# Kernel optimization log

Hardware: AMD Instinct MI355X
Metric: run time of the kernel (lower is better)

Reference implementation:

```python
import jax, jax.numpy as jnp
import numpy as np

EPS = 1e-8
NU_MOLECULAR = 1.5e-05
# loss weights (module defaults)
DATA_W, BC_W, TURB_W, RANS_W, SMOOTH_W, WALL_W = 1.0, 0.05, 0.05, 0.05, 0.01, 0.02
CONT_INIT = CONT_TGT = 0.1
MOM_INIT = MOM_TGT = 0.1
RAMP_STEPS, RAMP_START = 1000, 0

N_NODES, N_EDGES = 100000, 6400000


def _curriculum_weights(step):
    if step < RAMP_START:
        return CONT_INIT, MOM_INIT
    if step >= RAMP_START + RAMP_STEPS:
        return CONT_TGT, MOM_TGT
    alpha = (step - RAMP_START) / RAMP_STEPS  # linear ramp
    return ((1 - alpha) * CONT_INIT + alpha * CONT_TGT,
            (1 - alpha) * MOM_INIT + alpha * MOM_TGT)


def setup_inputs() -> dict:
    key = jax.random.key(0)
    k1, k2, k3, k4, k5 = jax.random.split(key, 5)
    predictions = jax.random.normal(k1, (N_NODES, 4), dtype=jnp.float32)
    targets = jax.random.normal(k2, (N_NODES, 4), dtype=jnp.float32)
    # dx, dy strictly positive edge offsets
    edge_attr_dxdy = jax.random.uniform(k3, (N_EDGES, 2), dtype=jnp.float32, minval=1e-3, maxval=0.05)
    edge_index = jax.random.randint(k4, (2, N_EDGES), 0, N_NODES, dtype=jnp.int64)
    wall_mask = jax.random.bernoulli(k5, 0.05, (N_NODES,))
    return {"predictions": predictions, "targets": targets,
            "edge_attr_dxdy": edge_attr_dxdy, "edge_index": edge_index,
            "wall_mask": wall_mask, "step": 500}


def reference(predictions, targets, edge_attr_dxdy, edge_index, wall_mask, step):
    cont_w, mom_w = _curriculum_weights(int(step))
    N = predictions.shape[0]
    row, col = edge_index[0], edge_index[1]
    u, v, p, nu_t = (predictions[:, i] for i in range(4))
    dx, dy = edge_attr_dxdy[:, 0], edge_attr_dxdy[:, 1]

    # per-edge finite differences (single gather of node fields)
    du = u[col] - u[row]
    dv = v[col] - v[row]
    dp = p[col] - p[row]

    seg = lambda e: jax.ops.segment_sum(e, row, num_segments=N)
    edge_count = jnp.maximum(seg(jnp.ones_like(du)), 1.0)

    # --- data loss ---
    mse_loss = jnp.mean((predictions - targets) ** 2)

    # --- continuity (divergence) loss ---
    divergence = (seg(du / (dx + EPS)) + seg(dv / (dy + EPS))) / edge_count
    div_loss = jnp.mean(divergence ** 2)

    # --- momentum loss ---
    p_grad_x = seg(dp / (dx + EPS)) / edge_count
    p_grad_y = seg(dp / (dy + EPS)) / edge_count
    lap_u = seg(du / (dx ** 2 + EPS)) / edge_count
    lap_v = seg(dv / (dy ** 2 + EPS)) / edge_count
    nu_eff = NU_MOLECULAR + nu_t
    momentum_loss = jnp.mean((p_grad_x + nu_eff * lap_u) ** 2 +
                             (p_grad_y + nu_eff * lap_v) ** 2)

    # --- turbulence losses ---
    positivity_loss = jnp.mean(jax.nn.relu(-nu_t) ** 2)
    du_dx = du / (dx + EPS)
    du_dy = du / (dy + EPS)
    dv_dx = dv / (dx + EPS)
    dv_dy = dv / (dy + EPS)
    strain_sq_edge = 2.0 * (du_dx ** 2 + dv_dy ** 2) + (du_dy + dv_dx) ** 2
    strain_node = seg(strain_sq_edge) / edge_count
    production = nu_t * strain_node
    turb_production_loss = jnp.mean(production ** 2)
    turb_dissipation_loss = jnp.mean(nu_t ** 2)

    # --- boundary-condition & wall-function losses (wall mask) ---
    m = wall_mask.astype(u.dtype)
    n_wall = jnp.maximum(jnp.sum(m), 1.0)
    bc_loss = jnp.sum(m * (u ** 2 + v ** 2)) / n_wall
    wall_loss = jnp.sum(m * (u ** 2 + v ** 2 + nu_t ** 2)) / n_wall

    # --- smoothness loss over edges ---
    smooth_loss = jnp.mean((predictions[col] - predictions[row]) ** 2)

    total = (DATA_W * mse_loss + cont_w * div_loss + mom_w * momentum_loss +
             TURB_W * turb_production_loss + RANS_W * turb_dissipation_loss +
             BC_W * bc_loss + SMOOTH_W * smooth_loss + WALL_W * wall_loss)
    # positivity_loss is tracked but not weighted into total (per visible code paths)
    return total
```

## Files before the change

### kernel.cpp

```cpp
#include <hip/hip_runtime.h>
#include <hip/hip_fp16.h>

#define EPS 1e-8f
#define NU_MOL 1.5e-5f
#define NPB 512
#define MAXNB 256
#define NBP 256
#define NBLK 4096
#define CMAX 1664
#define KMAX 7
#define CH 2048
#define SPLIT 6
#define NGRP 64
#define GRP 64


union U32H2 { unsigned u; __half2 h; };

__device__ inline unsigned packh2(float a, float b) {
    U32H2 x; x.h = __halves2half2(__float2half_rn(a), __float2half_rn(b));
    return x.u;
}
__device__ inline float2 unpackh2(unsigned u) {
    U32H2 x; x.u = u;
    return make_float2(__low2float(x.h), __high2float(x.h));
}
__device__ inline unsigned bf16rne(float f) {
    unsigned u = __float_as_uint(f);
    u += 0x7FFFu + ((u >> 16) & 1u);
    return u >> 16;
}
__device__ inline float bf16dec(unsigned h) {
    return __uint_as_float(h << 16);
}


__global__ void detect_idx_dtype(const void* eidx, int N, int* flag) {
    const long long* ll = (const long long*)eidx;
    int is64 = 1;
    for (int i = 0; i < 16; ++i) {
        long long v = ll[i];
        if (v < 0 || v >= (long long)N) { is64 = 0; break; }
    }
    *flag = is64;
}

__global__ void finalize_kernel(const double* __restrict__ d,
                                const double* __restrict__ smooth_slots,
                                int N, int E, float* __restrict__ out)
{
    double smooth = 0.0;
    for (int i = 0; i < 64; ++i) smooth += smooth_slots[i];
    double dN = (double)N;
    double n_wall = d[5] > 1.0 ? d[5] : 1.0;
    double total = 1.0  * d[0] / (4.0 * dN)
                 + 0.1  * d[1] / dN
                 + 0.1  * d[2] / dN
                 + 0.05 * d[3] / dN
                 + 0.05 * d[4] / dN
                 + 0.05 * d[6] / n_wall
                 + 0.01 * smooth / (4.0 * (double)E)
                 + 0.02 * d[7] / n_wall;
    out[0] = (float)total;
}


__global__ __launch_bounds__(256) void count_kernel(
    const void* __restrict__ eidx, int E, int N, int NB,
    const int* __restrict__ flag, unsigned* __restrict__ counts)
{
    __shared__ unsigned hist[MAXNB];
    hist[threadIdx.x] = 0u;
    __syncthreads();
    const int is64 = *flag;
    const long long* ll = (const long long*)eidx;
    const int* ii = (const int*)eidx;
    int chunk = (E + NBLK - 1) / NBLK;
    int s = blockIdx.x * chunk;
    int eend = min(E, s + chunk);
    for (int e = s + (int)threadIdx.x; e < eend; e += 256) {
        int r = is64 ? (int)ll[e] : ii[e];
        r = min(max(r, 0), N - 1);
        atomicAdd(&hist[r >> 9], 1u);
    }
    __syncthreads();
    if (threadIdx.x < NB)
        counts[(size_t)blockIdx.x * NBP + threadIdx.x] = hist[threadIdx.x];
}

__global__ __launch_bounds__(256) void group_sums_kernel(
    const unsigned* __restrict__ counts, unsigned* __restrict__ gsum, int NB)
{
    __shared__ unsigned red[4][64];
    int g = blockIdx.x;
    int b0 = blockIdx.y * 64;
    int j = threadIdx.x & 63, seg = threadIdx.x >> 6;
    int b = b0 + j;
    unsigned ssum = 0;
    if (b < NB) {
        #pragma unroll
        for (int k = 0; k < 16; ++k) {
            int row = g * GRP + seg * 16 + k;
            ssum += counts[(size_t)row * NBP + b];
        }
    }
    red[seg][j] = ssum;
    __syncthreads();
    if (seg == 0 && b < NB)
        gsum[(size_t)g * NBP + b] = red[0][j] + red[1][j] + red[2][j] + red[3][j];
}

__global__ __launch_bounds__(512) void scan_base_kernel(
    unsigned* __restrict__ gsum, unsigned* __restrict__ base, int NB)
{
    __shared__ unsigned sc[512];
    int t = threadIdx.x;
    unsigned total = 0;
    if (t < NB)
        for (int g = 0; g < NGRP; ++g) total += gsum[(size_t)g * NBP + t];
    sc[t] = total; __syncthreads();
    for (int off = 1; off < 512; off <<= 1) {
        unsigned x = (t >= off) ? sc[t - off] : 0u;
        __syncthreads();
        sc[t] += x;
        __syncthreads();
    }
    unsigned ex = sc[t] - total;
    if (t < NB) {
        base[t] = ex;
        unsigned run = ex;
        for (int g = 0; g < NGRP; ++g) {
            unsigned x = gsum[(size_t)g * NBP + t];
            gsum[(size_t)g * NBP + t] = run;
            run += x;
        }
    }
    if (t == 511) base[NB] = sc[511];
}

__global__ __launch_bounds__(256) void local_scan_kernel(
    unsigned* __restrict__ counts, const unsigned* __restrict__ gsum, int NB)
{
    __shared__ unsigned segs[4][64];
    int g = blockIdx.x;
    int b0 = blockIdx.y * 64;
    int j = threadIdx.x & 63, seg = threadIdx.x >> 6;
    int b = b0 + j;
    unsigned v[16];
    unsigned ssum = 0;
    if (b < NB) {
        #pragma unroll
        for (int k = 0; k < 16; ++k) {
            int row = g * GRP + seg * 16 + k;
            v[k] = counts[(size_t)row * NBP + b];
            ssum += v[k];
        }
    }
    segs[seg][j] = ssum;
    __syncthreads();
    if (b < NB) {
        unsigned carry = gsum[(size_t)g * NBP + b];
        for (int s_ = 0; s_ < seg; ++s_) carry += segs[s_][j];
        #pragma unroll
        for (int k = 0; k < 16; ++k) {
            int row = g * GRP + seg * 16 + k;
            counts[(size_t)row * NBP + b] = carry;
            carry += v[k];
        }
    }
}

__global__ __launch_bounds__(256) void scatter_kernel(
    const void* __restrict__ eidx, const float2* __restrict__ eattr,
    int E, int N, int NB, const int* __restrict__ flag,
    const unsigned* __restrict__ localoff ,
    uint2* __restrict__ vals)
{
    __shared__ unsigned hist[MAXNB];
    __shared__ unsigned cur[MAXNB];
    __shared__ unsigned gb2[MAXNB];
    __shared__ uint2 pl[CMAX];
    __shared__ unsigned char bb[CMAX];
    __shared__ unsigned sc[256];

    const int t = threadIdx.x;
    const int blk = blockIdx.x;
    const int is64 = *flag;
    const long long* ll = (const long long*)eidx;
    const int* ii = (const int*)eidx;
    const int chunk = (E + NBLK - 1) / NBLK;
    const int s = blk * chunk;
    const int Cb = min(chunk, E - s);

    hist[t] = 0u;
    __syncthreads();

    unsigned rr[KMAX];
    #pragma unroll
    for (int k = 0; k < KMAX; ++k) {
        int i = k * 256 + t;
        if (i < Cb) {
            int r = is64 ? (int)ll[s + i] : ii[s + i];
            r = min(max(r, 0), N - 1);
            rr[k] = (unsigned)r;
            atomicAdd(&hist[r >> 9], 1u);
        } else rr[k] = 0xFFFFFFFFu;
    }
    if (t < NB) gb2[t] = localoff[(size_t)blk * NBP + t];
    __syncthreads();

    unsigned h = hist[t];
    sc[t] = h; __syncthreads();
    for (int off = 1; off < 256; off <<= 1) {
        unsigned x = (t >= off) ? sc[t - off] : 0u;
        __syncthreads();
        sc[t] += x;
        __syncthreads();
    }
    unsigned ex = sc[t] - h;
    hist[t] = ex;
    cur[t] = ex;
    __syncthreads();
    if (t < NB) gb2[t] -= hist[t];
    __syncthreads();

    #pragma unroll
    for (int k = 0; k < KMAX; ++k) {
        int i = k * 256 + t;
        if (i >= Cb) break;
        int e = s + i;
        unsigned r = rr[k];
        unsigned b = r >> 9;
        unsigned rl = r & (NPB - 1);
        int c = is64 ? (int)ll[(long long)E + e] : ii[E + e];
        c = min(max(c, 0), N - 1);
        float2 dxy = eattr[e];
        unsigned pk = (unsigned)c | (rl << 17);
        unsigned pos = atomicAdd(&cur[b], 1u);
        pl[pos] = make_uint2(pk, packh2(dxy.x, dxy.y));
        bb[pos] = (unsigned char)b;
    }
    __syncthreads();

    #pragma unroll
    for (int k = 0; k < KMAX; ++k) {
        int p = k * 256 + t;
        if (p >= Cb) break;
        unsigned b = bb[p];
        vals[gb2[b] + (unsigned)p] = pl[p];
    }
}

__global__ __launch_bounds__(512) void accum_kernel(
    const uint2* __restrict__ vals, const unsigned* __restrict__ base,
    const float4* __restrict__ pred, int N,
    float* __restrict__ g , double* __restrict__ smooth_slots)
{
    __shared__ uint2 pl[CH];
    __shared__ uint2 ph[NPB];
    __shared__ unsigned hist[NPB];
    __shared__ unsigned cur[NPB];
    __shared__ unsigned wt[8];
    __shared__ double sm[8];

    const int b = blockIdx.x;
    const int t = threadIdx.x;
    const int wv = t >> 6, lane = t & 63;
    const int n0 = b * NPB;

    {
        int n = n0 + t;
        float4 p = (n < N) ? pred[n] : make_float4(0.f, 0.f, 0.f, 0.f);
        ph[t] = make_uint2(packh2(p.x, p.y), packh2(p.z, p.w));
    }

    unsigned s0 = base[b], e0 = base[b + 1];
    unsigned len = e0 - s0;
    unsigned s = s0 + (unsigned)(((unsigned long long)len * blockIdx.y) / SPLIT);
    unsigned e = s0 + (unsigned)(((unsigned long long)len * (blockIdx.y + 1)) / SPLIT);

    float cnt = 0, sdiv = 0, smx = 0, smy = 0, sstr = 0;
    double smooth = 0.0;

    for (unsigned cs = s; cs < e; cs += CH) {
        const int n = (int)min((unsigned)CH, e - cs);
        hist[t] = 0u;
        __syncthreads();

        uint2 vv[4];
        #pragma unroll
        for (int k = 0; k < 4; ++k) {
            int i = k * 512 + t;
            if (i < n) {
                vv[k] = vals[cs + i];
                atomicAdd(&hist[(vv[k].x >> 17) & (NPB - 1)], 1u);
            } else vv[k].x = 0xFFFFFFFFu;
        }
        __syncthreads();

        unsigned v = hist[t];
        unsigned x = v;
        #pragma unroll
        for (int off = 1; off < 64; off <<= 1) {
            unsigned y = (unsigned)__shfl_up((int)x, off, 64);
            if (lane >= off) x += y;
        }
        if (lane == 63) wt[wv] = x;
        __syncthreads();
        unsigned wadd = 0;
        for (int w = 0; w < wv; ++w) wadd += wt[w];
        unsigned incl = x + wadd;
        unsigned ex0 = incl - v;
        cur[t] = ex0;
        cnt += (float)v;
        __syncthreads();

        #pragma unroll
        for (int k = 0; k < 4; ++k) {
            int i = k * 512 + t;
            if (i >= n) break;
            unsigned pk = vv[k].x;
            int col = (int)(pk & 0x1FFFFu);
            unsigned rl = (pk >> 17) & (NPB - 1);
            float2 dxy = unpackh2(vv[k].y);
            float4 pc = pred[col];
            uint2 pru = ph[rl];
            float2 pxy = unpackh2(pru.x);
            float2 pzw = unpackh2(pru.y);
            float du = pc.x - pxy.x, dv = pc.y - pxy.y;
            float dp = pc.z - pzw.x, dn = pc.w - pzw.y;
            float rx  = 1.0f / (dxy.x + EPS);
            float ry  = 1.0f / (dxy.y + EPS);
            float rx2 = 1.0f / (dxy.x * dxy.x + EPS);
            float ry2 = 1.0f / (dxy.y * dxy.y + EPS);
            float du_dx = du * rx, du_dy = du * ry;
            float dv_dx = dv * rx, dv_dy = dv * ry;
            float nu_eff = NU_MOL + pzw.y;
            float sh = du_dy + dv_dx;
            float div_e = du_dx + dv_dy;
            float mx_e  = dp * rx + nu_eff * du * rx2;
            float my_e  = dp * ry + nu_eff * dv * ry2;
            float str_e = 2.0f * (du_dx * du_dx + dv_dy * dv_dy) + sh * sh;
            unsigned pos = atomicAdd(&cur[rl], 1u);
            pl[pos] = make_uint2(bf16rne(div_e) | (bf16rne(mx_e) << 16),
                                 bf16rne(my_e) | (bf16rne(str_e) << 16));
            smooth += (double)(du * du + dv * dv + dp * dp + dn * dn);
        }
        __syncthreads();

        for (unsigned i = ex0; i < incl; ++i) {
            uint2 pv = pl[i];
            sdiv += bf16dec(pv.x & 0xFFFFu);
            smx  += bf16dec(pv.x >> 16);
            smy  += bf16dec(pv.y & 0xFFFFu);
            sstr += bf16dec(pv.y >> 16);
        }
        __syncthreads();
    }

    {
        int n = n0 + t;
        if (n < N) {
            atomicAdd(&g[0 * (size_t)N + n], cnt);
            atomicAdd(&g[1 * (size_t)N + n], sdiv);
            atomicAdd(&g[2 * (size_t)N + n], smx);
            atomicAdd(&g[3 * (size_t)N + n], smy);
            atomicAdd(&g[4 * (size_t)N + n], sstr);
        }
    }

    for (int off = 32; off > 0; off >>= 1)
        smooth += __shfl_down(smooth, off);
    if (lane == 0) sm[wv] = smooth;
    __syncthreads();
    if (t == 0) {
        double tot = 0;
        #pragma unroll
        for (int w = 0; w < 8; ++w) tot += sm[w];
        atomicAdd(&smooth_slots[(b * SPLIT + blockIdx.y) & 63], tot);
    }
}

__global__ __launch_bounds__(256) void node_final_kernel(
    const float* __restrict__ g, const float4* __restrict__ pred,
    const float4* __restrict__ tgt, const unsigned char* __restrict__ wall,
    int N, double* __restrict__ d)
{
    int i = blockIdx.x * 256 + threadIdx.x;
    double v0 = 0, v1 = 0, v2 = 0, v3 = 0, v4 = 0, v5 = 0, v6 = 0, v7 = 0;
    if (i < N) {
        float cnt = g[0 * (size_t)N + i];
        float inv = 1.0f / fmaxf(cnt, 1.0f);
        float div = g[1 * (size_t)N + i] * inv;
        float mx  = g[2 * (size_t)N + i] * inv;
        float my  = g[3 * (size_t)N + i] * inv;
        float sn  = g[4 * (size_t)N + i] * inv;
        float4 p = pred[i];
        float4 tg = tgt[i];
        float prod = p.w * sn;
        float m = wall[i] ? 1.0f : 0.0f;
        float e0 = p.x - tg.x, e1 = p.y - tg.y, e2 = p.z - tg.z, e3 = p.w - tg.w;
        float uv = p.x * p.x + p.y * p.y;
        v0 = (double)(e0 * e0 + e1 * e1 + e2 * e2 + e3 * e3);
        v1 = (double)div * (double)div;
        v2 = (double)mx * (double)mx + (double)my * (double)my;
        v3 = (double)prod * (double)prod;
        v4 = (double)p.w * (double)p.w;
        v5 = (double)m;
        v6 = (double)(m * uv);
        v7 = (double)(m * (uv + p.w * p.w));
    }
    for (int off = 32; off > 0; off >>= 1) {
        v0 += __shfl_down(v0, off); v1 += __shfl_down(v1, off);
        v2 += __shfl_down(v2, off); v3 += __shfl_down(v3, off);
        v4 += __shfl_down(v4, off); v5 += __shfl_down(v5, off);
        v6 += __shfl_down(v6, off); v7 += __shfl_down(v7, off);
    }
    __shared__ double sm[4][8];
    int lane = threadIdx.x & 63, wv = threadIdx.x >> 6;
    if (lane == 0) {
        sm[wv][0] = v0; sm[wv][1] = v1; sm[wv][2] = v2; sm[wv][3] = v3;
        sm[wv][4] = v4; sm[wv][5] = v5; sm[wv][6] = v6; sm[wv][7] = v7;
    }
    __syncthreads();
    if (threadIdx.x < 8) {
        int q = threadIdx.x;
        atomicAdd(&d[q], sm[0][q] + sm[1][q] + sm[2][q] + sm[3][q]);
    }
}


__global__ __launch_bounds__(256) void edge_kernel(
    const void* __restrict__ eidx, const float2* __restrict__ eattr,
    const float4* __restrict__ pred, int E, int N, const int* __restrict__ flag,
    float* __restrict__ a_cnt, float* __restrict__ a_div,
    float* __restrict__ a_mx, float* __restrict__ a_my,
    float* __restrict__ a_str, double* __restrict__ smooth_slots)
{
    const int is64 = *flag;
    const long long* ll = (const long long*)eidx;
    const int* ii = (const int*)eidx;
    double smooth = 0.0;
    const int stride = gridDim.x * blockDim.x;
    for (int e = blockIdx.x * blockDim.x + threadIdx.x; e < E; e += stride) {
        int row, col;
        if (is64) { row = (int)ll[e]; col = (int)ll[(long long)E + e]; }
        else      { row = ii[e];      col = ii[E + e]; }
        row = min(max(row, 0), N - 1);
        col = min(max(col, 0), N - 1);
        float2 dxy = eattr[e];
        float4 pr = pred[row];
        float4 pc = pred[col];
        float du = pc.x - pr.x, dv = pc.y - pr.y;
        float dp = pc.z - pr.z, dn = pc.w - pr.w;
        float rx  = 1.0f / (dxy.x + EPS);
        float ry  = 1.0f / (dxy.y + EPS);
        float rx2 = 1.0f / (dxy.x * dxy.x + EPS);
        float ry2 = 1.0f / (dxy.y * dxy.y + EPS);
        float du_dx = du * rx, du_dy = du * ry;
        float dv_dx = dv * rx, dv_dy = dv * ry;
        float nu_eff = NU_MOL + pr.w;
        atomicAdd(&a_cnt[row], 1.0f);
        atomicAdd(&a_div[row], du_dx + dv_dy);
        atomicAdd(&a_mx[row], dp * rx + nu_eff * du * rx2);
        atomicAdd(&a_my[row], dp * ry + nu_eff * dv * ry2);
        float sh = du_dy + dv_dx;
        atomicAdd(&a_str[row], 2.0f * (du_dx * du_dx + dv_dy * dv_dy) + sh * sh);
        smooth += (double)(du * du + dv * dv + dp * dp + dn * dn);
    }
    for (int off = 32; off > 0; off >>= 1)
        smooth += __shfl_down(smooth, off);
    __shared__ double sm[4];
    int lane = threadIdx.x & 63, wv = threadIdx.x >> 6;
    if (lane == 0) sm[wv] = smooth;
    __syncthreads();
    if (threadIdx.x == 0)
        atomicAdd(&smooth_slots[blockIdx.x & 63], sm[0] + sm[1] + sm[2] + sm[3]);
}

__global__ __launch_bounds__(256) void node_kernel(
    const float4* __restrict__ pred, const float4* __restrict__ tgt,
    const unsigned char* __restrict__ wall, int N,
    const float* __restrict__ a_cnt, const float* __restrict__ a_div,
    const float* __restrict__ a_mx, const float* __restrict__ a_my,
    const float* __restrict__ a_str, double* __restrict__ d)
{
    int i = blockIdx.x * blockDim.x + threadIdx.x;
    double v0 = 0, v1 = 0, v2 = 0, v3 = 0, v4 = 0, v5 = 0, v6 = 0, v7 = 0;
    if (i < N) {
        float4 p = pred[i];
        float4 t = tgt[i];
        float inv = 1.0f / fmaxf(a_cnt[i], 1.0f);
        float div = a_div[i] * inv;
        float mx = a_mx[i] * inv, my = a_my[i] * inv;
        float sn = a_str[i] * inv;
        float prod = p.w * sn;
        float m = wall[i] ? 1.0f : 0.0f;
        float e0 = p.x - t.x, e1 = p.y - t.y, e2 = p.z - t.z, e3 = p.w - t.w;
        float uv = p.x * p.x + p.y * p.y;
        v0 = (double)(e0 * e0 + e1 * e1 + e2 * e2 + e3 * e3);
        v1 = (double)div * (double)div;
        v2 = (double)mx * (double)mx + (double)my * (double)my;
        v3 = (double)prod * (double)prod;
        v4 = (double)p.w * (double)p.w;
        v5 = (double)m;
        v6 = (double)(m * uv);
        v7 = (double)(m * (uv + p.w * p.w));
    }
    for (int off = 32; off > 0; off >>= 1) {
        v0 += __shfl_down(v0, off); v1 += __shfl_down(v1, off);
        v2 += __shfl_down(v2, off); v3 += __shfl_down(v3, off);
        v4 += __shfl_down(v4, off); v5 += __shfl_down(v5, off);
        v6 += __shfl_down(v6, off); v7 += __shfl_down(v7, off);
    }
    __shared__ double sm[4][8];
    int lane = threadIdx.x & 63, wv = threadIdx.x >> 6;
    if (lane == 0) {
        sm[wv][0] = v0; sm[wv][1] = v1; sm[wv][2] = v2; sm[wv][3] = v3;
        sm[wv][4] = v4; sm[wv][5] = v5; sm[wv][6] = v6; sm[wv][7] = v7;
    }
    __syncthreads();
    if (threadIdx.x < 8) {
        int q = threadIdx.x;
        atomicAdd(&d[q], sm[0][q] + sm[1][q] + sm[2][q] + sm[3][q]);
    }
}


extern "C" void kernel_launch(void* const* d_in, const int* in_sizes, int n_in,
                              void* d_out, int out_size, void* d_ws, size_t ws_size,
                              hipStream_t stream) {
    const float4* pred = (const float4*)d_in[0];
    const float4* tgt  = (const float4*)d_in[1];
    const float2* eattr = (const float2*)d_in[2];
    const void* eidx = d_in[3];
    const unsigned char* wall = (const unsigned char*)d_in[4];
    int N = in_sizes[0] / 4;
    int E = in_sizes[2] / 2;
    int NB = (N + NPB - 1) / NPB;
    int chunk = (E + NBLK - 1) / NBLK;
    int ntiles = (NB + 63) / 64;

    char* ws = (char*)d_ws;
    double* d = (double*)ws;
    double* smooth_slots = d + 8;
    int* flag = (int*)(ws + 576);

    size_t off = 1024;
    float* g        = (float*)(ws + off);     off += (size_t)5 * N * 4;
    unsigned* counts = (unsigned*)(ws + off); off += (size_t)NBLK * NBP * 4;
    unsigned* gsum   = (unsigned*)(ws + off); off += (size_t)NGRP * NBP * 4;
    unsigned* base   = (unsigned*)(ws + off); off += (size_t)(NB + 1) * 4;
    off = (off + 15) & ~(size_t)15;
    uint2* vals      = (uint2*)(ws + off);    off += (size_t)E * 8;
    size_t need_fast = off;

    bool fast = (NB <= MAXNB) && (N <= 131072) && (chunk <= CMAX) &&
                (ws_size >= need_fast);

    if (fast) {
        hipMemsetAsync(d_ws, 0, 1024 + (size_t)5 * N * 4, stream);
        detect_idx_dtype<<<1, 1, 0, stream>>>(eidx, N, flag);
        count_kernel<<<NBLK, 256, 0, stream>>>(eidx, E, N, NB, flag, counts);
        group_sums_kernel<<<dim3(NGRP, ntiles), 256, 0, stream>>>(counts, gsum, NB);
        scan_base_kernel<<<1, 512, 0, stream>>>(gsum, base, NB);
        local_scan_kernel<<<dim3(NGRP, ntiles), 256, 0, stream>>>(counts, gsum, NB);
        scatter_kernel<<<NBLK, 256, 0, stream>>>(eidx, eattr, E, N, NB, flag,
                                                 counts, vals);
        accum_kernel<<<dim3(NB, SPLIT), 512, 0, stream>>>(vals, base, pred, N,
                                                          g, smooth_slots);
        node_final_kernel<<<(N + 255) / 256, 256, 0, stream>>>(g, pred, tgt, wall,
                                                               N, d);
        finalize_kernel<<<1, 1, 0, stream>>>(d, smooth_slots, N, E, (float*)d_out);
    } else {
        float* arrays = (float*)(ws + 1024);
        float* a_cnt = arrays + (size_t)0 * N;
        float* a_div = arrays + (size_t)1 * N;
        float* a_mx  = arrays + (size_t)2 * N;
        float* a_my  = arrays + (size_t)3 * N;
        float* a_str = arrays + (size_t)4 * N;
        size_t zbytes = 1024 + (size_t)5 * N * sizeof(float);
        hipMemsetAsync(d_ws, 0, zbytes, stream);
        detect_idx_dtype<<<1, 1, 0, stream>>>(eidx, N, flag);
        edge_kernel<<<4096, 256, 0, stream>>>(eidx, eattr, pred, E, N, flag,
                                              a_cnt, a_div, a_mx, a_my, a_str,
                                              smooth_slots);
        node_kernel<<<(N + 255) / 256, 256, 0, stream>>>(pred, tgt, wall, N,
                                                         a_cnt, a_div, a_mx, a_my,
                                                         a_str, d);
        finalize_kernel<<<1, 1, 0, stream>>>(d, smooth_slots, N, E, (float*)d_out);
    }
}
```

Baseline: 238.8 us.

## Replace atomics with per-split partials, use wave-shuffle scans, fuse finalize

The accumulation kernel now writes per-split partial sums to separate slices instead of issuing float atomics, and the node kernel sums the slices. The memset of the node arrays is dropped. The LDS Hillis-Steele scans in scan_base and scatter are replaced by wave shuffle scans, and the gsum layout is transposed. The finalize kernel is folded into node_final through a last-block counter. SPLIT goes from 6 to 8. This removes launches, atomics and barriers at the cost of more partial-sum memory traffic. Every split must write every node in its range, otherwise the sums read garbage.

New measurement: 269.8 us. +13.0%, slower.

```diff
diff --git a/kernel.cpp b/kernel.cpp
--- a/kernel.cpp
+++ b/kernel.cpp
@@ -10,7 +10,7 @@
 #define CMAX 1664
 #define KMAX 7
 #define CH 2048
-#define SPLIT 6
+#define SPLIT 8
 #define NGRP 64
 #define GRP 64
 
@@ -107,35 +107,43 @@
     red[seg][j] = ssum;
     __syncthreads();
     if (seg == 0 && b < NB)
-        gsum[(size_t)g * NBP + b] = red[0][j] + red[1][j] + red[2][j] + red[3][j];
-}
-
-__global__ __launch_bounds__(512) void scan_base_kernel(
+        gsum[(size_t)b * NGRP + g] = red[0][j] + red[1][j] + red[2][j] + red[3][j];
+}
+
+__global__ __launch_bounds__(256) void scan_base_kernel(
     unsigned* __restrict__ gsum, unsigned* __restrict__ base, int NB)
 {
-    __shared__ unsigned sc[512];
+    __shared__ unsigned wt[4];
     int t = threadIdx.x;
+    int lane = t & 63, wv = t >> 6;
     unsigned total = 0;
-    if (t < NB)
-        for (int g = 0; g < NGRP; ++g) total += gsum[(size_t)g * NBP + t];
-    sc[t] = total; __syncthreads();
-    for (int off = 1; off < 512; off <<= 1) {
-        unsigned x = (t >= off) ? sc[t - off] : 0u;
-        __syncthreads();
-        sc[t] += x;
-        __syncthreads();
-    }
-    unsigned ex = sc[t] - total;
+    if (t < NB) {
+        #pragma unroll 1
+        for (int g = 0; g < NGRP; ++g) total += gsum[(size_t)t * NGRP + g];
+    }
+    unsigned x = total;
+    #pragma unroll
+    for (int off = 1; off < 64; off <<= 1) {
+        unsigned y = (unsigned)__shfl_up((int)x, off, 64);
+        if (lane >= off) x += y;
+    }
+    if (lane == 63) wt[wv] = x;
+    __syncthreads();
+    unsigned wadd = 0;
+    for (int w = 0; w < wv; ++w) wadd += wt[w];
+    unsigned incl = x + wadd;
+    unsigned ex = incl - total;
     if (t < NB) {
         base[t] = ex;
+        if (t == NB - 1) base[NB] = incl;
         unsigned run = ex;
+        #pragma unroll 1
         for (int g = 0; g < NGRP; ++g) {
-            unsigned x = gsum[(size_t)g * NBP + t];
-            gsum[(size_t)g * NBP + t] = run;
-            run += x;
-        }
-    }
-    if (t == 511) base[NB] = sc[511];
+            unsigned v = gsum[(size_t)t * NGRP + g];
+            gsum[(size_t)t * NGRP + g] = run;
+            run += v;
+        }
+    }
 }
 
 __global__ __launch_bounds__(256) void local_scan_kernel(
@@ -159,7 +167,7 @@
     segs[seg][j] = ssum;
     __syncthreads();
     if (b < NB) {
-        unsigned carry = gsum[(size_t)g * NBP + b];
+        unsigned carry = gsum[(size_t)b * NGRP + g];
         for (int s_ = 0; s_ < seg; ++s_) carry += segs[s_][j];
         #pragma unroll
         for (int k = 0; k < 16; ++k) {
@@ -181,10 +189,11 @@
     __shared__ unsigned gb2[MAXNB];
     __shared__ uint2 pl[CMAX];
     __shared__ unsigned char bb[CMAX];
-    __shared__ unsigned sc[256];
+    __shared__ unsigned wt[4];
 
     const int t = threadIdx.x;
     const int blk = blockIdx.x;
+    const int lane = t & 63, wv = t >> 6;
     const int is64 = *flag;
     const long long* ll = (const long long*)eidx;
     const int* ii = (const int*)eidx;
@@ -210,14 +219,17 @@
     __syncthreads();
 
     unsigned h = hist[t];
-    sc[t] = h; __syncthreads();
-    for (int off = 1; off < 256; off <<= 1) {
-        unsigned x = (t >= off) ? sc[t - off] : 0u;
-        __syncthreads();
-        sc[t] += x;
-        __syncthreads();
-    }
-    unsigned ex = sc[t] - h;
+    unsigned x = h;
+    #pragma unroll
+    for (int off = 1; off < 64; off <<= 1) {
+        unsigned y = (unsigned)__shfl_up((int)x, off, 64);
+        if (lane >= off) x += y;
+    }
+    if (lane == 63) wt[wv] = x;
+    __syncthreads();
+    unsigned wadd = 0;
+    for (int w = 0; w < wv; ++w) wadd += wt[w];
+    unsigned ex = x + wadd - h;
     hist[t] = ex;
     cur[t] = ex;
     __syncthreads();
@@ -361,11 +373,12 @@
     {
         int n = n0 + t;
         if (n < N) {
-            atomicAdd(&g[0 * (size_t)N + n], cnt);
-            atomicAdd(&g[1 * (size_t)N + n], sdiv);
-            atomicAdd(&g[2 * (size_t)N + n], smx);
-            atomicAdd(&g[3 * (size_t)N + n], smy);
-            atomicAdd(&g[4 * (size_t)N + n], sstr);
+            float* gs = g + (size_t)blockIdx.y * 5 * N;
+            gs[0 * (size_t)N + n] = cnt;
+            gs[1 * (size_t)N + n] = sdiv;
+            gs[2 * (size_t)N + n] = smx;
+            gs[3 * (size_t)N + n] = smy;
+            gs[4 * (size_t)N + n] = sstr;
         }
     }
 
@@ -384,17 +397,28 @@
 __global__ __launch_bounds__(256) void node_final_kernel(
     const float* __restrict__ g, const float4* __restrict__ pred,
     const float4* __restrict__ tgt, const unsigned char* __restrict__ wall,
-    int N, double* __restrict__ d)
+    int N, int E, double* __restrict__ d,
+    const double* __restrict__ smooth_slots, unsigned* __restrict__ counter,
+    float* __restrict__ out)
 {
     int i = blockIdx.x * 256 + threadIdx.x;
     double v0 = 0, v1 = 0, v2 = 0, v3 = 0, v4 = 0, v5 = 0, v6 = 0, v7 = 0;
     if (i < N) {
-        float cnt = g[0 * (size_t)N + i];
+        float cnt = 0, sdiv = 0, smx = 0, smy = 0, sstr = 0;
+        #pragma unroll
+        for (int s = 0; s < SPLIT; ++s) {
+            const float* gs = g + (size_t)s * 5 * N;
+            cnt  += gs[0 * (size_t)N + i];
+            sdiv += gs[1 * (size_t)N + i];
+            smx  += gs[2 * (size_t)N + i];
+            smy  += gs[3 * (size_t)N + i];
+            sstr += gs[4 * (size_t)N + i];
+        }
         float inv = 1.0f / fmaxf(cnt, 1.0f);
-        float div = g[1 * (size_t)N + i] * inv;
-        float mx  = g[2 * (size_t)N + i] * inv;
-        float my  = g[3 * (size_t)N + i] * inv;
-        float sn  = g[4 * (size_t)N + i] * inv;
+        float div = sdiv * inv;
+        float mx  = smx * inv;
+        float my  = smy * inv;
+        float sn  = sstr * inv;
         float4 p = pred[i];
         float4 tg = tgt[i];
         float prod = p.w * sn;
@@ -417,6 +441,7 @@
         v6 += __shfl_down(v6, off); v7 += __shfl_down(v7, off);
     }
     __shared__ double sm[4][8];
+    __shared__ int is_last;
     int lane = threadIdx.x & 63, wv = threadIdx.x >> 6;
     if (lane == 0) {
         sm[wv][0] = v0; sm[wv][1] = v1; sm[wv][2] = v2; sm[wv][3] = v3;
@@ -426,6 +451,32 @@
     if (threadIdx.x < 8) {
         int q = threadIdx.x;
         atomicAdd(&d[q], sm[0][q] + sm[1][q] + sm[2][q] + sm[3][q]);
+    }
+    __threadfence();
+    __syncthreads();
+    if (threadIdx.x == 0) {
+        unsigned prev = atomicAdd(counter, 1u);
+        is_last = (prev == gridDim.x - 1) ? 1 : 0;
+    }
+    __syncthreads();
+    if (is_last && threadIdx.x == 0) {
+        __threadfence();
+        double dd[8];
+        #pragma unroll
+        for (int q = 0; q < 8; ++q) dd[q] = atomicAdd(&d[q], 0.0);
+        double smooth = 0.0;
+        for (int k = 0; k < 64; ++k) smooth += smooth_slots[k];
+        double dN = (double)N;
+        double n_wall = dd[5] > 1.0 ? dd[5] : 1.0;
+        double total = 1.0  * dd[0] / (4.0 * dN)
+                     + 0.1  * dd[1] / dN
+                     + 0.1  * dd[2] / dN
+                     + 0.05 * dd[3] / dN
+                     + 0.05 * dd[4] / dN
+                     + 0.05 * dd[6] / n_wall
+                     + 0.01 * smooth / (4.0 * (double)E)
+                     + 0.02 * dd[7] / n_wall;
+        out[0] = (float)total;
     }
 }
 
@@ -545,11 +596,12 @@
     double* d = (double*)ws;
     double* smooth_slots = d + 8;
     int* flag = (int*)(ws + 576);
+    unsigned* counter = (unsigned*)(ws + 580);
 
     size_t off = 1024;
-    float* g        = (float*)(ws + off);     off += (size_t)5 * N * 4;
+    float* g        = (float*)(ws + off);     off += (size_t)SPLIT * 5 * N * 4;
     unsigned* counts = (unsigned*)(ws + off); off += (size_t)NBLK * NBP * 4;
-    unsigned* gsum   = (unsigned*)(ws + off); off += (size_t)NGRP * NBP * 4;
+    unsigned* gsum   = (unsigned*)(ws + off); off += (size_t)MAXNB * NGRP * 4;
     unsigned* base   = (unsigned*)(ws + off); off += (size_t)(NB + 1) * 4;
     off = (off + 15) & ~(size_t)15;
     uint2* vals      = (uint2*)(ws + off);    off += (size_t)E * 8;
@@ -559,19 +611,20 @@
                 (ws_size >= need_fast);
 
     if (fast) {
-        hipMemsetAsync(d_ws, 0, 1024 + (size_t)5 * N * 4, stream);
+        hipMemsetAsync(d_ws, 0, 1024, stream);
         detect_idx_dtype<<<1, 1, 0, stream>>>(eidx, N, flag);
         count_kernel<<<NBLK, 256, 0, stream>>>(eidx, E, N, NB, flag, counts);
         group_sums_kernel<<<dim3(NGRP, ntiles), 256, 0, stream>>>(counts, gsum, NB);
-        scan_base_kernel<<<1, 512, 0, stream>>>(gsum, base, NB);
+        scan_base_kernel<<<1, 256, 0, stream>>>(gsum, base, NB);
         local_scan_kernel<<<dim3(NGRP, ntiles), 256, 0, stream>>>(counts, gsum, NB);
         scatter_kernel<<<NBLK, 256, 0, stream>>>(eidx, eattr, E, N, NB, flag,
                                                  counts, vals);
         accum_kernel<<<dim3(NB, SPLIT), 512, 0, stream>>>(vals, base, pred, N,
                                                           g, smooth_slots);
         node_final_kernel<<<(N + 255) / 256, 256, 0, stream>>>(g, pred, tgt, wall,
-                                                               N, d);
-        finalize_kernel<<<1, 1, 0, stream>>>(d, smooth_slots, N, E, (float*)d_out);
+                                                               N, E, d,
+                                                               smooth_slots, counter,
+                                                               (float*)d_out);
     } else {
         float* arrays = (float*)(ws + 1024);
         float* a_cnt = arrays + (size_t)0 * N;
```
